# Kernel optimization log

Measured on AMD Instinct MI355X. Metric: run time of the kernel, lower is better.

## Reference

```python
import jax, jax.numpy as jnp
import numpy as np

D_MODEL = 1024
D_INNER = 2048  # expand * d_model
D_STATE = 16
D_CONV = 4
DT_RANK = 64    # ceil(d_model / 16)
B_SZ, L_SEQ = 2, 1024


def setup_inputs() -> dict:
    key = jax.random.key(0)
    ks = jax.random.split(key, 8)
    s = lambda fan_in: 1.0 / np.sqrt(fan_in)
    x = jax.random.normal(ks[0], (B_SZ, L_SEQ, D_MODEL), dtype=jnp.float32)
    in_proj_w = jax.random.normal(ks[1], (2 * D_INNER, D_MODEL), jnp.float32) * s(D_MODEL)
    conv_w = jax.random.normal(ks[2], (D_INNER, 1, D_CONV), jnp.float32) * s(D_CONV)
    conv_b = jax.random.normal(ks[3], (D_INNER,), jnp.float32) * 0.02
    x_proj_w = jax.random.normal(ks[4], (DT_RANK + 2 * D_STATE, D_INNER), jnp.float32) * s(D_INNER)
    dt_proj_w = jax.random.normal(ks[5], (D_INNER, DT_RANK), jnp.float32) * s(DT_RANK)
    dt_proj_b = jax.random.normal(ks[6], (D_INNER,), jnp.float32) * 0.02
    A_log = jnp.broadcast_to(jnp.log(jnp.arange(1, D_STATE + 1, dtype=jnp.float32)), (D_INNER, D_STATE))
    D_param = jnp.ones((D_INNER,), jnp.float32)
    out_proj_w = jax.random.normal(ks[7], (D_MODEL, D_INNER), jnp.float32) * s(D_INNER)
    return dict(x=x, in_proj_w=in_proj_w, conv_w=conv_w, conv_b=conv_b,
                x_proj_w=x_proj_w, dt_proj_w=dt_proj_w, dt_proj_b=dt_proj_b,
                A_log=A_log, D_param=D_param, out_proj_w=out_proj_w)


def _mamba_forward(x, in_proj_w, conv_w, conv_b, x_proj_w, dt_proj_w, dt_proj_b, A_log, D_param, out_proj_w):
    B, L, _ = x.shape
    # in_proj: (B,L,2*d_inner) -> split into conv branch and gate
    xz = jnp.einsum('bld,ed->ble', x, in_proj_w)
    x_br, z = jnp.split(xz, 2, axis=-1)
    # depthwise causal conv1d (left pad d_conv-1, truncate to L == torch pad+slice)
    xc = jnp.transpose(x_br, (0, 2, 1))  # (B, d_inner, L)
    xc = jax.lax.conv_general_dilated(
        xc, conv_w, window_strides=(1,), padding=[(D_CONV - 1, 0)],
        dimension_numbers=('NCH', 'OIH', 'NCH'), feature_group_count=D_INNER)
    xc = xc + conv_b[None, :, None]
    u = jax.nn.silu(jnp.transpose(xc, (0, 2, 1)))  # (B, L, d_inner) = SSM input
    # input-dependent params
    proj = jnp.einsum('bld,ed->ble', u, x_proj_w)
    delta_raw, B_in, C_in = jnp.split(proj, [DT_RANK, DT_RANK + D_STATE], axis=-1)
    delta = jax.nn.softplus(jnp.einsum('blr,dr->bld', delta_raw, dt_proj_w) + dt_proj_b)
    A = -jnp.exp(A_log)  # (d_inner, d_state)

    def step(h, inp):
        d_t, b_t, c_t, u_t = inp  # (B,d_inner),(B,d_state),(B,d_state),(B,d_inner)
        dA = jnp.exp(d_t[:, :, None] * A)                       # (B,d_inner,d_state)
        h = dA * h + (d_t * u_t)[:, :, None] * b_t[:, None, :]  # ZOH-ish update
        y_t = jnp.einsum('bds,bs->bd', h, c_t) + D_param * u_t
        return h, y_t

    h0 = jnp.zeros((B, D_INNER, D_STATE), dtype=x.dtype)
    inputs = (jnp.swapaxes(delta, 0, 1), jnp.swapaxes(B_in, 0, 1),
              jnp.swapaxes(C_in, 0, 1), jnp.swapaxes(u, 0, 1))
    _, ys = jax.lax.scan(step, h0, inputs)  # (L, B, d_inner)
    y = jnp.swapaxes(ys, 0, 1) * jax.nn.silu(z)
    return jnp.einsum('ble,de->bld', y, out_proj_w)


def reference(x, in_proj_w, conv_w, conv_b, x_proj_w, dt_proj_w, dt_proj_b, A_log, D_param, out_proj_w):
    return _mamba_forward(x, in_proj_w, conv_w, conv_b, x_proj_w, dt_proj_w, dt_proj_b, A_log, D_param, out_proj_w)
```

## Files before the change

kernel.cpp:

```cpp
#include <hip/hip_runtime.h>
#include <hip/hip_bf16.h>

#define D_MODEL 1024
#define D_INNER 2048
#define D_STATE 16
#define D_CONV  4
#define DT_RANK 64
#define B_SZ    2
#define L_SEQ   1024
#define BL      (B_SZ * L_SEQ)
#define NPROJ   (DT_RANK + 2 * D_STATE)

typedef __attribute__((ext_vector_type(8))) short bf16x8;
typedef __attribute__((ext_vector_type(4))) float floatx4;
typedef unsigned short ushort_t;

__device__ __forceinline__ void mfma_bf16(floatx4& acc, bf16x8 a, bf16x8 b) {
    asm volatile("v_mfma_f32_16x16x32_bf16 %0, %1, %2, %0"
                 : "+v"(acc) : "v"(a), "v"(b));
}

__device__ __forceinline__ void cvt_hilo(float f, ushort_t& hi, ushort_t& lo) {
    __hip_bfloat16 h = __float2bfloat16(f);
    hi = *(ushort_t*)&h;
    __hip_bfloat16 l = __float2bfloat16(f - __bfloat162float(h));
    lo = *(ushort_t*)&l;
}

__device__ __forceinline__ void cvt_store4(float4 v, ushort_t* hi, ushort_t* lo) {
    ushort4 h, l;
    cvt_hilo(v.x, h.x, l.x);
    cvt_hilo(v.y, h.y, l.y);
    cvt_hilo(v.z, h.z, l.z);
    cvt_hilo(v.w, h.w, l.w);
    *(ushort4*)hi = h;
    *(ushort4*)lo = l;
}

#define N4_WI 1048576
#define N4_WO 524288
#define N4_X  524288
#define N4_WD 32768
#define N4_TOT  (N4_WI + N4_WO + N4_X + N4_WD)

__global__ __launch_bounds__(256) void cvt_static(
    const float* __restrict__ wi, ushort_t* wihi, ushort_t* wilo,
    const float* __restrict__ wo, ushort_t* wohi, ushort_t* wolo,
    const float* __restrict__ x,  ushort_t* xhi,  ushort_t* xlo,
    const float* __restrict__ wd, ushort_t* wdhi, ushort_t* wdlo)
{
    int i = blockIdx.x * 256 + threadIdx.x;
    if (i >= N4_TOT) return;
    const float* src; ushort_t *dh, *dl;
    if (i < N4_WI)                 { src = wi; dh = wihi; dl = wilo; }
    else if ((i -= N4_WI) < N4_WO) { src = wo; dh = wohi; dl = wolo; }
    else if ((i -= N4_WO) < N4_X)  { src = x;  dh = xhi;  dl = xlo;  }
    else                           { i -= N4_X; src = wd; dh = wdhi; dl = wdlo; }
    float4 v = ((const float4*)src)[i];
    cvt_store4(v, dh + i * 4, dl + i * 4);
}

template <int KSPLIT>
__global__ __launch_bounds__(512, 1) void gemm_big(
    const ushort_t* __restrict__ Ahi, const ushort_t* __restrict__ Alo, int lda,
    const ushort_t* __restrict__ Bhi, const ushort_t* __restrict__ Blo, int ldb,
    float* __restrict__ C, int ldc, int K, size_t cslice)
{
    constexpr int BM = 128, BN = 256, LDT = 32;
    __shared__ __align__(16) ushort_t As[3][2][BM * LDT];
    __shared__ __align__(16) ushort_t Bs[3][2][BN * LDT];

    const int tid = threadIdx.x;
    const int bm = blockIdx.y * BM;
    const int bn = blockIdx.x * BN;
    const int kstart = (KSPLIT > 1) ? blockIdx.z * (K / KSPLIT) : 0;
    const int nt = ((KSPLIT > 1) ? K / KSPLIT : K) >> 5;

    const int wave = tid >> 6;
    const int lane = tid & 63;
    const int wm = (wave >> 2) * 64;
    const int wn = (wave & 3) * 64;
    const int ml = lane & 15;
    const int q  = lane >> 4;

    const int rsub = lane >> 2;
    const int gg   = ((lane & 3) ^ ((lane >> 3) & 3)) * 8;
    const ushort_t* gsrc = Ahi; int grow0 = bm, gld = lda;
    if (wave == 1)      { gsrc = Alo; grow0 = bm;       gld = lda; }
    else if (wave == 2) { gsrc = Bhi; grow0 = bn;       gld = ldb; }
    else if (wave == 3) { gsrc = Bhi; grow0 = bn + 128; gld = ldb; }
    else if (wave == 4) { gsrc = Blo; grow0 = bn;       gld = ldb; }
    else if (wave == 5) { gsrc = Blo; grow0 = bn + 128; gld = ldb; }
    const bool do_stage = (wave < 6);

    auto stage = [&](int buf, int kc) {
        if (!do_stage) return;
        ushort_t* lb;
        if (wave == 0)      lb = &As[buf][0][0];
        else if (wave == 1) lb = &As[buf][1][0];
        else if (wave == 2) lb = &Bs[buf][0][0];
        else if (wave == 3) lb = &Bs[buf][0][128 * LDT];
        else if (wave == 4) lb = &Bs[buf][1][0];
        else                lb = &Bs[buf][1][128 * LDT];
#pragma unroll
        for (int u2 = 0; u2 < 8; ++u2) {
            const int R0 = u2 * 16;
            const ushort_t* src =
                gsrc + (size_t)(grow0 + R0 + rsub) * gld + kc + gg;
            __builtin_amdgcn_global_load_lds(
                (const __attribute__((address_space(1))) unsigned int*)src,
                (__attribute__((address_space(3))) unsigned int*)(lb + R0 * LDT),
                16, 0, 0);
        }
    };

    floatx4 acc[4][4];
#pragma unroll
    for (int i = 0; i < 4; ++i)
#pragma unroll
        for (int j = 0; j < 4; ++j) acc[i][j] = (floatx4)0.f;

    stage(0, kstart);
    if (nt > 1) stage(1, kstart + 32);

    for (int t = 0; t < nt; ++t) {
        asm volatile("s_waitcnt vmcnt(8)" ::: "memory");
        __builtin_amdgcn_s_barrier();
        if (t + 2 < nt) stage((t + 2) % 3, kstart + ((t + 2) << 5));

        const int buf = t % 3;
        bf16x8 ah[4], al[4], bh[4], bl[4];
#pragma unroll
        for (int i = 0; i < 4; ++i) {
            const int r = wm + i * 16 + ml;
            const int p = (q ^ ((r >> 1) & 3)) * 8;
            ah[i] = *(const bf16x8*)&As[buf][0][r * LDT + p];
            al[i] = *(const bf16x8*)&As[buf][1][r * LDT + p];
        }
#pragma unroll
        for (int j = 0; j < 4; ++j) {
            const int r = wn + j * 16 + ml;
            const int p = (q ^ ((r >> 1) & 3)) * 8;
            bh[j] = *(const bf16x8*)&Bs[buf][0][r * LDT + p];
            bl[j] = *(const bf16x8*)&Bs[buf][1][r * LDT + p];
        }
#pragma unroll
        for (int i = 0; i < 4; ++i)
#pragma unroll
            for (int j = 0; j < 4; ++j) {
                mfma_bf16(acc[i][j], ah[i], bh[j]);
                mfma_bf16(acc[i][j], ah[i], bl[j]);
                mfma_bf16(acc[i][j], al[i], bh[j]);
            }
    }

    asm volatile("s_nop 7\n\ts_nop 7\n\ts_nop 7" ::: "memory");

    float* Cb = (KSPLIT > 1) ? C + (size_t)blockIdx.z * cslice : C;
#pragma unroll
    for (int i = 0; i < 4; ++i)
#pragma unroll
        for (int j = 0; j < 4; ++j)
#pragma unroll
            for (int r = 0; r < 4; ++r) {
                const int row = bm + wm + i * 16 + q * 4 + r;
                const int col = bn + wn + j * 16 + ml;
                Cb[(size_t)row * ldc + col] = acc[i][j][r];
            }
}

template <int TM, int TN, int EPI>
__global__ __launch_bounds__(256, 2) void gemm_pre(
    const ushort_t* __restrict__ Ahi, const ushort_t* __restrict__ Alo, int lda,
    const ushort_t* __restrict__ Bhi, const ushort_t* __restrict__ Blo, int ldb,
    float* __restrict__ C, int ldc, int K,
    const float* __restrict__ bias)
{
    static_assert(TM == 128 && TN == 128, "stage mapping assumes 128x128");
    constexpr int LDT = 32;
    constexpr int IT = TM / 32, JT = TN / 32;
    __shared__ __align__(16) ushort_t As[2][2][TM * LDT];
    __shared__ __align__(16) ushort_t Bs[2][2][TN * LDT];

    const int tid = threadIdx.x;
    const int bm = blockIdx.y * TM;
    const int bn = blockIdx.x * TN;

    const int wave = tid >> 6;
    const int lane = tid & 63;
    const int wm = (wave >> 1) * (TM / 2);
    const int wn = (wave & 1) * (TN / 2);
    const int ml = lane & 15;
    const int q  = lane >> 4;

    const ushort_t* gplane = (wave == 0) ? Ahi : (wave == 1) ? Alo
                           : (wave == 2) ? Bhi : Blo;
    const int grow0 = (wave < 2) ? bm : bn;
    const int gld   = (wave < 2) ? lda : ldb;
    const int rsub  = lane >> 2;
    const int gg    = ((lane & 3) ^ ((lane >> 3) & 3)) * 8;

    auto stage = [&](int buf, int kc) {
        ushort_t* lbase = (wave < 2) ? &As[buf][wave & 1][0]
                                     : &Bs[buf][wave & 1][0];
#pragma unroll
        for (int u = 0; u < 8; ++u) {
            const int R0 = u * 16;
            const ushort_t* src =
                gplane + (size_t)(grow0 + R0 + rsub) * gld + kc + gg;
            __builtin_amdgcn_global_load_lds(
                (const __attribute__((address_space(1))) unsigned int*)src,
                (__attribute__((address_space(3))) unsigned int*)(lbase + R0 * LDT),
                16, 0, 0);
        }
    };

    floatx4 acc[IT][JT];
#pragma unroll
    for (int i = 0; i < IT; ++i)
#pragma unroll
        for (int j = 0; j < JT; ++j) acc[i][j] = (floatx4)0.f;

    const int nt = K >> 5;

    stage(0, 0);
    __syncthreads();

    for (int t = 0; t < nt; ++t) {
        const int buf = t & 1;
        if (t + 1 < nt) stage(buf ^ 1, (t + 1) << 5);

        bf16x8 ah[IT], al[IT], bh[JT], bl[JT];
#pragma unroll
        for (int i = 0; i < IT; ++i) {
            const int r = wm + i * 16 + ml;
            const int p = (q ^ ((r >> 1) & 3)) * 8;
            ah[i] = *(const bf16x8*)&As[buf][0][r * LDT + p];
            al[i] = *(const bf16x8*)&As[buf][1][r * LDT + p];
        }
#pragma unroll
        for (int j = 0; j < JT; ++j) {
            const int r = wn + j * 16 + ml;
            const int p = (q ^ ((r >> 1) & 3)) * 8;
            bh[j] = *(const bf16x8*)&Bs[buf][0][r * LDT + p];
            bl[j] = *(const bf16x8*)&Bs[buf][1][r * LDT + p];
        }
#pragma unroll
        for (int i = 0; i < IT; ++i)
#pragma unroll
            for (int j = 0; j < JT; ++j) {
                mfma_bf16(acc[i][j], ah[i], bh[j]);
                mfma_bf16(acc[i][j], ah[i], bl[j]);
                mfma_bf16(acc[i][j], al[i], bh[j]);
            }

        __syncthreads();
    }

    asm volatile("s_nop 7\n\ts_nop 7\n\ts_nop 7" ::: "memory");

#pragma unroll
    for (int i = 0; i < IT; ++i)
#pragma unroll
        for (int j = 0; j < JT; ++j) {
            const int col = bn + wn + j * 16 + ml;
            const float bv = (EPI == 1) ? bias[col] : 0.f;
#pragma unroll
            for (int r = 0; r < 4; ++r) {
                const int row = bm + wm + i * 16 + q * 4 + r;
                float v = acc[i][j][r];
                if (EPI == 1) {
                    v += bv;
                    v = (v > 20.f) ? v : log1pf(__expf(v));
                }
                C[(size_t)row * ldc + col] = v;
            }
        }
}

__global__ __launch_bounds__(256) void fold_out(
    const float* __restrict__ s, float* __restrict__ out)
{
    const int i = blockIdx.x * 256 + threadIdx.x;
    const float4* s4 = (const float4*)s;
    constexpr int SL = BL * D_MODEL / 4;
    float4 a = s4[i], b = s4[i + SL], c = s4[i + 2 * SL], d = s4[i + 3 * SL];
    ((float4*)out)[i] = make_float4(a.x + b.x + c.x + d.x,
                                    a.y + b.y + c.y + d.y,
                                    a.z + b.z + c.z + d.z,
                                    a.w + b.w + c.w + d.w);
}

__global__ __launch_bounds__(256) void fold_proj(
    const float* __restrict__ pp, float* __restrict__ proj,
    ushort_t* __restrict__ Phi, ushort_t* __restrict__ Plo)
{
    const int i = blockIdx.x * 256 + threadIdx.x;
    constexpr int SL = BL * NPROJ / 4;
    float4 acc = make_float4(0.f, 0.f, 0.f, 0.f);
#pragma unroll
    for (int sp = 0; sp < 16; ++sp) {
        float4 v = ((const float4*)pp)[i + sp * SL];
        acc.x += v.x; acc.y += v.y; acc.z += v.z; acc.w += v.w;
    }
    ((float4*)proj)[i] = acc;

    const int row = i / (NPROJ / 4);
    const int c4  = i % (NPROJ / 4);
    if (c4 < DT_RANK / 4)
        cvt_store4(acc, Phi + (size_t)row * DT_RANK + c4 * 4,
                        Plo + (size_t)row * DT_RANK + c4 * 4);
}

#define PKC 128
#define PSC 64

__global__ __launch_bounds__(256) void gemm_proj_conv(
    const float* __restrict__ xz,
    const float* __restrict__ conv_w,
    const float* __restrict__ conv_b,
    const float* __restrict__ Wp,
    float* __restrict__ projp,
    float* __restrict__ u_out)
{
    __shared__ float us[PSC][65];
    __shared__ float wsh[PSC][100];

    const int tid = threadIdx.x;
    const int bm = blockIdx.y * 64;
    const int kbase0 = blockIdx.x * PKC;

    const int tx = tid & 15;
    const int ty = tid >> 4;

    float acc[4][6];
#pragma unroll
    for (int i = 0; i < 4; ++i)
#pragma unroll
        for (int j = 0; j < 6; ++j) acc[i][j] = 0.f;

    for (int sc = 0; sc < PKC / PSC; ++sc) {
        const int kb = kbase0 + sc * PSC;
        __syncthreads();
#pragma unroll
        for (int i = 0; i < 4; ++i) {
            const int flat = tid + 256 * i;
            const int r  = flat >> 4;
            const int kk = (flat & 15) * 4;
            const int k  = kb + kk;
            const int rr = bm + r;
            const int t  = rr & (L_SEQ - 1);
            const float* base = xz + (size_t)rr * 4096 + k;
            float4 x0 = *(const float4*)(base);
            float4 x1 = (t >= 1) ? *(const float4*)(base - 4096)  : make_float4(0,0,0,0);
            float4 x2 = (t >= 2) ? *(const float4*)(base - 8192)  : make_float4(0,0,0,0);
            float4 x3 = (t >= 3) ? *(const float4*)(base - 12288) : make_float4(0,0,0,0);
            float4 cb = *(const float4*)(conv_b + k);
            float4 w0 = ((const float4*)conv_w)[k + 0];
            float4 w1 = ((const float4*)conv_w)[k + 1];
            float4 w2 = ((const float4*)conv_w)[k + 2];
            float4 w3 = ((const float4*)conv_w)[k + 3];
            float4 uo;
            { float a = cb.x + w0.x*x3.x + w0.y*x2.x + w0.z*x1.x + w0.w*x0.x;
              uo.x = a / (1.f + __expf(-a)); }
            { float a = cb.y + w1.x*x3.y + w1.y*x2.y + w1.z*x1.y + w1.w*x0.y;
              uo.y = a / (1.f + __expf(-a)); }
            { float a = cb.z + w2.x*x3.z + w2.y*x2.z + w2.z*x1.z + w2.w*x0.z;
              uo.z = a / (1.f + __expf(-a)); }
            { float a = cb.w + w3.x*x3.w + w3.y*x2.w + w3.z*x1.w + w3.w*x0.w;
              uo.w = a / (1.f + __expf(-a)); }
            us[kk + 0][r] = uo.x;
            us[kk + 1][r] = uo.y;
            us[kk + 2][r] = uo.z;
            us[kk + 3][r] = uo.w;
            *(float4*)(u_out + (size_t)rr * D_INNER + k) = uo;
        }
#pragma unroll
        for (int i = 0; i < 6; ++i) {
            const int flat = tid + 256 * i;
            const int r = flat >> 4;
            const int k4 = flat & 15;
            float4 v = *(const float4*)(Wp + (size_t)r * D_INNER + kb + k4 * 4);
            wsh[k4*4+0][r] = v.x; wsh[k4*4+1][r] = v.y;
            wsh[k4*4+2][r] = v.z; wsh[k4*4+3][r] = v.w;
        }
        __syncthreads();

#pragma unroll 8
        for (int kk = 0; kk < PSC; ++kk) {
            float a[4], b[6];
#pragma unroll
            for (int i = 0; i < 4; ++i) a[i] = us[kk][ty * 4 + i];
#pragma unroll
            for (int j = 0; j < 6; ++j) b[j] = wsh[kk][tx + 16 * j];
#pragma unroll
            for (int i = 0; i < 4; ++i)
#pragma unroll
                for (int j = 0; j < 6; ++j) acc[i][j] += a[i] * b[j];
        }
    }

    float* pb = projp + (size_t)blockIdx.x * (BL * NPROJ);
#pragma unroll
    for (int i = 0; i < 4; ++i)
#pragma unroll
        for (int j = 0; j < 6; ++j)
            pb[(size_t)(bm + ty * 4 + i) * NPROJ + tx + 16 * j] = acc[i][j];
}

template <int CSv>
__global__ __launch_bounds__(256) void scan_phase_a(
    const float* __restrict__ xz,
    const float* __restrict__ u,
    const float* __restrict__ proj,
    const float* __restrict__ A_log,
    float* __restrict__ hloc,
    float* __restrict__ sumd,
    int nc)
{
    const int d = blockIdx.x * 256 + threadIdx.x;
    const int c = blockIdx.y;
    const int b = blockIdx.z;

    float a[D_STATE];
#pragma unroll
    for (int s = 0; s < D_STATE; ++s) a[s] = -__expf(A_log[d * D_STATE + s]);

    float h[D_STATE];
#pragma unroll
    for (int s = 0; s < D_STATE; ++s) h[s] = 0.f;
    float sd = 0.f;

    for (int t = c * CSv; t < (c + 1) * CSv; ++t) {
        const size_t bt = (size_t)b * L_SEQ + t;
        const float dv = xz[bt * (2 * D_INNER) + d];
        const float uv = u[bt * D_INNER + d];
        const float du = dv * uv;
        sd += dv;
        const float* pr = proj + bt * NPROJ;
#pragma unroll
        for (int s = 0; s < D_STATE; ++s)
            h[s] = __expf(dv * a[s]) * h[s] + du * pr[DT_RANK + s];
    }

    const size_t base = ((size_t)(b * nc + c) * D_STATE) * D_INNER + d;
#pragma unroll
    for (int s = 0; s < D_STATE; ++s) hloc[base + (size_t)s * D_INNER] = h[s];
    sumd[(size_t)(b * nc + c) * D_INNER + d] = sd;
}

__global__ __launch_bounds__(256) void scan_phase_b(
    const float* __restrict__ hloc,
    const float* __restrict__ sumd,
    const float* __restrict__ A_log,
    float* __restrict__ carry,
    int nc)
{
    const int g = blockIdx.x * 256 + threadIdx.x;
    const int d = g & (D_INNER - 1);
    const int s = (g >> 11) & (D_STATE - 1);
    const int b = g >> 15;

    const float a_s = -__expf(A_log[d * D_STATE + s]);

    float hc = 0.f;
    carry[((size_t)(b * nc + 0) * D_STATE + s) * D_INNER + d] = 0.f;

    for (int c = 1; c < nc; ++c) {
        const float sd = sumd[(size_t)(b * nc + c - 1) * D_INNER + d];
        const float hl = hloc[((size_t)(b * nc + c - 1) * D_STATE + s) * D_INNER + d];
        hc = __expf(a_s * sd) * hc + hl;
        carry[((size_t)(b * nc + c) * D_STATE + s) * D_INNER + d] = hc;
    }
}

template <int CSv>
__global__ __launch_bounds__(256) void scan_phase_c(
    const float* __restrict__ xz,
    const float* __restrict__ u,
    const float* __restrict__ proj,
    const float* __restrict__ A_log,
    const float* __restrict__ D_param,
    const float* __restrict__ carry,
    ushort_t* __restrict__ Yhi,
    ushort_t* __restrict__ Ylo,
    int nc)
{
    const int d = blockIdx.x * 256 + threadIdx.x;
    const int c = blockIdx.y;
    const int b = blockIdx.z;

    float a[D_STATE];
#pragma unroll
    for (int s = 0; s < D_STATE; ++s) a[s] = -__expf(A_log[d * D_STATE + s]);
    const float Dp = D_param[d];

    float h[D_STATE];
    const size_t cbase = ((size_t)(b * nc + c) * D_STATE) * D_INNER + d;
#pragma unroll
    for (int s = 0; s < D_STATE; ++s) h[s] = carry[cbase + (size_t)s * D_INNER];

    for (int t = c * CSv; t < (c + 1) * CSv; ++t) {
        const size_t bt = (size_t)b * L_SEQ + t;
        const float dv = xz[bt * (2 * D_INNER) + d];
        const float uv = u[bt * D_INNER + d];
        const float du = dv * uv;
        const float* pr = proj + bt * NPROJ;

        float acc = 0.f;
#pragma unroll
        for (int s = 0; s < D_STATE; ++s) {
            h[s] = __expf(dv * a[s]) * h[s] + du * pr[DT_RANK + s];
            acc += h[s] * pr[DT_RANK + D_STATE + s];
        }
        const float yv = acc + Dp * uv;

        const float zv = xz[bt * (2 * D_INNER) + D_INNER + d];
        const float gate = zv / (1.f + __expf(-zv));
        ushort_t hh, ll;
        cvt_hilo(yv * gate, hh, ll);
        Yhi[bt * D_INNER + d] = hh;
        Ylo[bt * D_INNER + d] = ll;
    }
}

extern "C" void kernel_launch(void* const* d_in, const int* in_sizes, int n_in,
                              void* d_out, int out_size, void* d_ws, size_t ws_size,
                              hipStream_t stream)
{
    const float* x         = (const float*)d_in[0];
    const float* in_proj_w = (const float*)d_in[1];
    const float* conv_w    = (const float*)d_in[2];
    const float* conv_b    = (const float*)d_in[3];
    const float* x_proj_w  = (const float*)d_in[4];
    const float* dt_proj_w = (const float*)d_in[5];
    const float* dt_proj_b = (const float*)d_in[6];
    const float* A_log     = (const float*)d_in[7];
    const float* D_param   = (const float*)d_in[8];
    const float* out_proj_w= (const float*)d_in[9];
    float* out = (float*)d_out;

    const size_t fixed =
        (size_t)BL * 4096 * 4 +
        (size_t)BL * 2048 * 4 +
        (size_t)BL * NPROJ * 4 +
        (size_t)(4096 + 2048) * 1024 * 2 * 2;
    const size_t need64 = fixed + (size_t)B_SZ * 64 * D_INNER * 4
                                + (size_t)B_SZ * 64 * D_STATE * D_INNER * 4;
    const int nc = (ws_size >= need64) ? 64 : 32;
    const int cs = L_SEQ / nc;

    float* xz    = (float*)d_ws;
    float* u     = xz    + (size_t)BL * 4096;
    float* proj  = u     + (size_t)BL * 2048;
    float* sumd  = proj  + (size_t)BL * NPROJ;
    float* carry = sumd  + (size_t)B_SZ * nc * D_INNER;
    ushort_t* Wihi = (ushort_t*)(carry + (size_t)B_SZ * nc * D_STATE * D_INNER);
    ushort_t* Wilo = Wihi + (size_t)4096 * 1024;
    ushort_t* Wohi = Wilo + (size_t)4096 * 1024;
    ushort_t* Wolo = Wohi + (size_t)1024 * 2048;
    ushort_t* Xhi  = (ushort_t*)carry;
    ushort_t* Xlo  = Xhi + (size_t)BL * D_MODEL;
    float*    hloc = (float*)Wihi;
    ushort_t* Yhi  = Wihi;
    ushort_t* Ylo  = Wilo;
    float*    projp = (float*)Wihi;
    ushort_t* Phi  = Xhi;
    ushort_t* Plo  = Xhi + (size_t)BL * DT_RANK;
    ushort_t* Wdhi = (ushort_t*)sumd;
    ushort_t* Wdlo = Wdhi + (size_t)D_INNER * DT_RANK;
    float*    Cslc  = xz;

    dim3 blk(256);
    dim3 blk512(512);

    cvt_static<<<(N4_TOT + 255) / 256, blk, 0, stream>>>(
        in_proj_w, Wihi, Wilo, out_proj_w, Wohi, Wolo, x, Xhi, Xlo,
        dt_proj_w, Wdhi, Wdlo);

    gemm_big<1><<<dim3(4096 / 256, BL / 128), blk512, 0, stream>>>(
        Xhi, Xlo, D_MODEL, Wihi, Wilo, D_MODEL, xz, 2 * D_INNER, D_MODEL, 0);

    gemm_proj_conv<<<dim3(D_INNER / PKC, BL / 64), blk, 0, stream>>>(
        xz, conv_w, conv_b, x_proj_w, projp, u);

    fold_proj<<<(BL * NPROJ / 4) / 256, blk, 0, stream>>>(projp, proj, Phi, Plo);

    gemm_pre<128, 128, 1><<<dim3(D_INNER / 128, BL / 128), blk, 0, stream>>>(
        Phi, Plo, DT_RANK, Wdhi, Wdlo, DT_RANK, xz, 2 * D_INNER, DT_RANK,
        dt_proj_b);

    if (cs == 16) {
        scan_phase_a<16><<<dim3(D_INNER / 256, nc, B_SZ), blk, 0, stream>>>(
            xz, u, proj, A_log, hloc, sumd, nc);
    } else {
        scan_phase_a<32><<<dim3(D_INNER / 256, nc, B_SZ), blk, 0, stream>>>(
            xz, u, proj, A_log, hloc, sumd, nc);
    }
    scan_phase_b<<<dim3((B_SZ * D_INNER * D_STATE) / 256), blk, 0, stream>>>(
        hloc, sumd, A_log, carry, nc);
    if (cs == 16) {
        scan_phase_c<16><<<dim3(D_INNER / 256, nc, B_SZ), blk, 0, stream>>>(
            xz, u, proj, A_log, D_param, carry, Yhi, Ylo, nc);
    } else {
        scan_phase_c<32><<<dim3(D_INNER / 256, nc, B_SZ), blk, 0, stream>>>(
            xz, u, proj, A_log, D_param, carry, Yhi, Ylo, nc);
    }

    gemm_big<4><<<dim3(D_MODEL / 256, BL / 128, 4), blk512, 0, stream>>>(
        Yhi, Ylo, D_INNER, Wohi, Wolo, D_INNER, Cslc, D_MODEL, D_INNER,
        (size_t)BL * D_MODEL);
    fold_out<<<(BL * D_MODEL / 4) / 256, blk, 0, stream>>>(Cslc, out);
}
```

Before: 295.0 us.

## Fuse dt_proj GEMM and softplus into scan phases, drop separate GEMM

Removes the split-bf16 dt_proj GEMM kernel, its weight and activation conversions, and the delta write to the xz buffer. Both scan phases now compute delta per thread in fp32 as a 64-wide dot product with dt_proj_w held in registers, then apply softplus. This saves a kernel launch and the delta round trip through global memory. In exchange the dt_proj matmul is done twice (in phase A and phase C) on plain FMA units, and register pressure rises (64 weights plus CSv deltas), with launch bounds set to 4 blocks per CU.

New measurement: 337.9 us. 1.15x slower.

```diff
diff --git a/kernel.cpp b/kernel.cpp
--- a/kernel.cpp
+++ b/kernel.cpp
@@ -40,22 +40,19 @@
 #define N4_WI 1048576
 #define N4_WO 524288
 #define N4_X  524288
-#define N4_WD 32768
-#define N4_TOT  (N4_WI + N4_WO + N4_X + N4_WD)
+#define N4_TOT  (N4_WI + N4_WO + N4_X)
 
 __global__ __launch_bounds__(256) void cvt_static(
     const float* __restrict__ wi, ushort_t* wihi, ushort_t* wilo,
     const float* __restrict__ wo, ushort_t* wohi, ushort_t* wolo,
-    const float* __restrict__ x,  ushort_t* xhi,  ushort_t* xlo,
-    const float* __restrict__ wd, ushort_t* wdhi, ushort_t* wdlo)
+    const float* __restrict__ x,  ushort_t* xhi,  ushort_t* xlo)
 {
     int i = blockIdx.x * 256 + threadIdx.x;
     if (i >= N4_TOT) return;
     const float* src; ushort_t *dh, *dl;
     if (i < N4_WI)                 { src = wi; dh = wihi; dl = wilo; }
     else if ((i -= N4_WI) < N4_WO) { src = wo; dh = wohi; dl = wolo; }
-    else if ((i -= N4_WO) < N4_X)  { src = x;  dh = xhi;  dl = xlo;  }
-    else                           { i -= N4_X; src = wd; dh = wdhi; dl = wdlo; }
+    else                           { i -= N4_WO; src = x; dh = xhi; dl = xlo; }
     float4 v = ((const float4*)src)[i];
     cvt_store4(v, dh + i * 4, dl + i * 4);
 }
@@ -169,115 +166,6 @@
             }
 }
 
-template <int TM, int TN, int EPI>
-__global__ __launch_bounds__(256, 2) void gemm_pre(
-    const ushort_t* __restrict__ Ahi, const ushort_t* __restrict__ Alo, int lda,
-    const ushort_t* __restrict__ Bhi, const ushort_t* __restrict__ Blo, int ldb,
-    float* __restrict__ C, int ldc, int K,
-    const float* __restrict__ bias)
-{
-    static_assert(TM == 128 && TN == 128, "stage mapping assumes 128x128");
-    constexpr int LDT = 32;
-    constexpr int IT = TM / 32, JT = TN / 32;
-    __shared__ __align__(16) ushort_t As[2][2][TM * LDT];
-    __shared__ __align__(16) ushort_t Bs[2][2][TN * LDT];
-
-    const int tid = threadIdx.x;
-    const int bm = blockIdx.y * TM;
-    const int bn = blockIdx.x * TN;
-
-    const int wave = tid >> 6;
-    const int lane = tid & 63;
-    const int wm = (wave >> 1) * (TM / 2);
-    const int wn = (wave & 1) * (TN / 2);
-    const int ml = lane & 15;
-    const int q  = lane >> 4;
-
-    const ushort_t* gplane = (wave == 0) ? Ahi : (wave == 1) ? Alo
-                           : (wave == 2) ? Bhi : Blo;
-    const int grow0 = (wave < 2) ? bm : bn;
-    const int gld   = (wave < 2) ? lda : ldb;
-    const int rsub  = lane >> 2;
-    const int gg    = ((lane & 3) ^ ((lane >> 3) & 3)) * 8;
-
-    auto stage = [&](int buf, int kc) {
-        ushort_t* lbase = (wave < 2) ? &As[buf][wave & 1][0]
-                                     : &Bs[buf][wave & 1][0];
-#pragma unroll
-        for (int u = 0; u < 8; ++u) {
-            const int R0 = u * 16;
-            const ushort_t* src =
-                gplane + (size_t)(grow0 + R0 + rsub) * gld + kc + gg;
-            __builtin_amdgcn_global_load_lds(
-                (const __attribute__((address_space(1))) unsigned int*)src,
-                (__attribute__((address_space(3))) unsigned int*)(lbase + R0 * LDT),
-                16, 0, 0);
-        }
-    };
-
-    floatx4 acc[IT][JT];
-#pragma unroll
-    for (int i = 0; i < IT; ++i)
-#pragma unroll
-        for (int j = 0; j < JT; ++j) acc[i][j] = (floatx4)0.f;
-
-    const int nt = K >> 5;
-
-    stage(0, 0);
-    __syncthreads();
-
-    for (int t = 0; t < nt; ++t) {
-        const int buf = t & 1;
-        if (t + 1 < nt) stage(buf ^ 1, (t + 1) << 5);
-
-        bf16x8 ah[IT], al[IT], bh[JT], bl[JT];
-#pragma unroll
-        for (int i = 0; i < IT; ++i) {
-            const int r = wm + i * 16 + ml;
-            const int p = (q ^ ((r >> 1) & 3)) * 8;
-            ah[i] = *(const bf16x8*)&As[buf][0][r * LDT + p];
-            al[i] = *(const bf16x8*)&As[buf][1][r * LDT + p];
-        }
-#pragma unroll
-        for (int j = 0; j < JT; ++j) {
-            const int r = wn + j * 16 + ml;
-            const int p = (q ^ ((r >> 1) & 3)) * 8;
-            bh[j] = *(const bf16x8*)&Bs[buf][0][r * LDT + p];
-            bl[j] = *(const bf16x8*)&Bs[buf][1][r * LDT + p];
-        }
-#pragma unroll
-        for (int i = 0; i < IT; ++i)
-#pragma unroll
-            for (int j = 0; j < JT; ++j) {
-                mfma_bf16(acc[i][j], ah[i], bh[j]);
-                mfma_bf16(acc[i][j], ah[i], bl[j]);
-                mfma_bf16(acc[i][j], al[i], bh[j]);
-            }
-
-        __syncthreads();
-    }
-
-    asm volatile("s_nop 7\n\ts_nop 7\n\ts_nop 7" ::: "memory");
-
-#pragma unroll
-    for (int i = 0; i < IT; ++i)
-#pragma unroll
-        for (int j = 0; j < JT; ++j) {
-            const int col = bn + wn + j * 16 + ml;
-            const float bv = (EPI == 1) ? bias[col] : 0.f;
-#pragma unroll
-            for (int r = 0; r < 4; ++r) {
-                const int row = bm + wm + i * 16 + q * 4 + r;
-                float v = acc[i][j][r];
-                if (EPI == 1) {
-                    v += bv;
-                    v = (v > 20.f) ? v : log1pf(__expf(v));
-                }
-                C[(size_t)row * ldc + col] = v;
-            }
-        }
-}
-
 __global__ __launch_bounds__(256) void fold_out(
     const float* __restrict__ s, float* __restrict__ out)
 {
@@ -292,8 +180,7 @@
 }
 
 __global__ __launch_bounds__(256) void fold_proj(
-    const float* __restrict__ pp, float* __restrict__ proj,
-    ushort_t* __restrict__ Phi, ushort_t* __restrict__ Plo)
+    const float* __restrict__ pp, float* __restrict__ proj)
 {
     const int i = blockIdx.x * 256 + threadIdx.x;
     constexpr int SL = BL * NPROJ / 4;
@@ -304,12 +191,6 @@
         acc.x += v.x; acc.y += v.y; acc.z += v.z; acc.w += v.w;
     }
     ((float4*)proj)[i] = acc;
-
-    const int row = i / (NPROJ / 4);
-    const int c4  = i % (NPROJ / 4);
-    if (c4 < DT_RANK / 4)
-        cvt_store4(acc, Phi + (size_t)row * DT_RANK + c4 * 4,
-                        Plo + (size_t)row * DT_RANK + c4 * 4);
 }
 
 #define PKC 128
@@ -409,10 +290,11 @@
 }
 
 template <int CSv>
-__global__ __launch_bounds__(256) void scan_phase_a(
-    const float* __restrict__ xz,
+__global__ __launch_bounds__(256, 4) void scan_phase_a(
     const float* __restrict__ u,
     const float* __restrict__ proj,
+    const float* __restrict__ Wd,
+    const float* __restrict__ dbias,
     const float* __restrict__ A_log,
     float* __restrict__ hloc,
     float* __restrict__ sumd,
@@ -422,6 +304,33 @@
     const int c = blockIdx.y;
     const int b = blockIdx.z;
 
+    float dloc[CSv];
+    float sd = 0.f;
+    {
+        float w[64];
+#pragma unroll
+        for (int k4 = 0; k4 < 16; ++k4) {
+            float4 v = *(const float4*)(Wd + (size_t)d * 64 + k4 * 4);
+            w[k4*4+0] = v.x; w[k4*4+1] = v.y; w[k4*4+2] = v.z; w[k4*4+3] = v.w;
+        }
+        const float bv = dbias[d];
+#pragma unroll
+        for (int tt = 0; tt < CSv; ++tt) {
+            const size_t bt = (size_t)b * L_SEQ + c * CSv + tt;
+            const float* pr = proj + bt * NPROJ;
+            float dr = bv;
+#pragma unroll
+            for (int k4 = 0; k4 < 16; ++k4) {
+                float4 p = *(const float4*)(pr + k4 * 4);
+                dr += p.x * w[k4*4+0] + p.y * w[k4*4+1]
+                    + p.z * w[k4*4+2] + p.w * w[k4*4+3];
+            }
+            const float dv = (dr > 20.f) ? dr : log1pf(__expf(dr));
+            dloc[tt] = dv;
+            sd += dv;
+        }
+    }
+
     float a[D_STATE];
 #pragma unroll
     for (int s = 0; s < D_STATE; ++s) a[s] = -__expf(A_log[d * D_STATE + s]);
@@ -429,14 +338,13 @@
     float h[D_STATE];
 #pragma unroll
     for (int s = 0; s < D_STATE; ++s) h[s] = 0.f;
-    float sd = 0.f;
-
-    for (int t = c * CSv; t < (c + 1) * CSv; ++t) {
-        const size_t bt = (size_t)b * L_SEQ + t;
-        const float dv = xz[bt * (2 * D_INNER) + d];
+
+#pragma unroll
+    for (int tt = 0; tt < CSv; ++tt) {
+        const size_t bt = (size_t)b * L_SEQ + c * CSv + tt;
+        const float dv = dloc[tt];
         const float uv = u[bt * D_INNER + d];
         const float du = dv * uv;
-        sd += dv;
         const float* pr = proj + bt * NPROJ;
 #pragma unroll
         for (int s = 0; s < D_STATE; ++s)
@@ -475,10 +383,12 @@
 }
 
 template <int CSv>
-__global__ __launch_bounds__(256) void scan_phase_c(
+__global__ __launch_bounds__(256, 4) void scan_phase_c(
     const float* __restrict__ xz,
     const float* __restrict__ u,
     const float* __restrict__ proj,
+    const float* __restrict__ Wd,
+    const float* __restrict__ dbias,
     const float* __restrict__ A_log,
     const float* __restrict__ D_param,
     const float* __restrict__ carry,
@@ -490,6 +400,30 @@
     const int c = blockIdx.y;
     const int b = blockIdx.z;
 
+    float dloc[CSv];
+    {
+        float w[64];
+#pragma unroll
+        for (int k4 = 0; k4 < 16; ++k4) {
+            float4 v = *(const float4*)(Wd + (size_t)d * 64 + k4 * 4);
+            w[k4*4+0] = v.x; w[k4*4+1] = v.y; w[k4*4+2] = v.z; w[k4*4+3] = v.w;
+        }
+        const float bv = dbias[d];
+#pragma unroll
+        for (int tt = 0; tt < CSv; ++tt) {
+            const size_t bt = (size_t)b * L_SEQ + c * CSv + tt;
+            const float* pr = proj + bt * NPROJ;
+            float dr = bv;
+#pragma unroll
+            for (int k4 = 0; k4 < 16; ++k4) {
+                float4 p = *(const float4*)(pr + k4 * 4);
+                dr += p.x * w[k4*4+0] + p.y * w[k4*4+1]
+                    + p.z * w[k4*4+2] + p.w * w[k4*4+3];
+            }
+            dloc[tt] = (dr > 20.f) ? dr : log1pf(__expf(dr));
+        }
+    }
+
     float a[D_STATE];
 #pragma unroll
     for (int s = 0; s < D_STATE; ++s) a[s] = -__expf(A_log[d * D_STATE + s]);
@@ -500,9 +434,10 @@
 #pragma unroll
     for (int s = 0; s < D_STATE; ++s) h[s] = carry[cbase + (size_t)s * D_INNER];
 
-    for (int t = c * CSv; t < (c + 1) * CSv; ++t) {
-        const size_t bt = (size_t)b * L_SEQ + t;
-        const float dv = xz[bt * (2 * D_INNER) + d];
+#pragma unroll
+    for (int tt = 0; tt < CSv; ++tt) {
+        const size_t bt = (size_t)b * L_SEQ + c * CSv + tt;
+        const float dv = dloc[tt];
         const float uv = u[bt * D_INNER + d];
         const float du = dv * uv;
         const float* pr = proj + bt * NPROJ;
@@ -565,18 +500,13 @@
     ushort_t* Yhi  = Wihi;
     ushort_t* Ylo  = Wilo;
     float*    projp = (float*)Wihi;
-    ushort_t* Phi  = Xhi;
-    ushort_t* Plo  = Xhi + (size_t)BL * DT_RANK;
-    ushort_t* Wdhi = (ushort_t*)sumd;
-    ushort_t* Wdlo = Wdhi + (size_t)D_INNER * DT_RANK;
     float*    Cslc  = xz;
 
     dim3 blk(256);
     dim3 blk512(512);
 
     cvt_static<<<(N4_TOT + 255) / 256, blk, 0, stream>>>(
-        in_proj_w, Wihi, Wilo, out_proj_w, Wohi, Wolo, x, Xhi, Xlo,
-        dt_proj_w, Wdhi, Wdlo);
+        in_proj_w, Wihi, Wilo, out_proj_w, Wohi, Wolo, x, Xhi, Xlo);
 
     gemm_big<1><<<dim3(4096 / 256, BL / 128), blk512, 0, stream>>>(
         Xhi, Xlo, D_MODEL, Wihi, Wilo, D_MODEL, xz, 2 * D_INNER, D_MODEL, 0);
@@ -584,27 +514,25 @@
     gemm_proj_conv<<<dim3(D_INNER / PKC, BL / 64), blk, 0, stream>>>(
         xz, conv_w, conv_b, x_proj_w, projp, u);
 
-    fold_proj<<<(BL * NPROJ / 4) / 256, blk, 0, stream>>>(projp, proj, Phi, Plo);
-
-    gemm_pre<128, 128, 1><<<dim3(D_INNER / 128, BL / 128), blk, 0, stream>>>(
-        Phi, Plo, DT_RANK, Wdhi, Wdlo, DT_RANK, xz, 2 * D_INNER, DT_RANK,
-        dt_proj_b);
+    fold_proj<<<(BL * NPROJ / 4) / 256, blk, 0, stream>>>(projp, proj);
 
     if (cs == 16) {
         scan_phase_a<16><<<dim3(D_INNER / 256, nc, B_SZ), blk, 0, stream>>>(
-            xz, u, proj, A_log, hloc, sumd, nc);
+            u, proj, dt_proj_w, dt_proj_b, A_log, hloc, sumd, nc);
     } else {
         scan_phase_a<32><<<dim3(D_INNER / 256, nc, B_SZ), blk, 0, stream>>>(
-            xz, u, proj, A_log, hloc, sumd, nc);
+            u, proj, dt_proj_w, dt_proj_b, A_log, hloc, sumd, nc);
     }
     scan_phase_b<<<dim3((B_SZ * D_INNER * D_STATE) / 256), blk, 0, stream>>>(
         hloc, sumd, A_log, carry, nc);
     if (cs == 16) {
         scan_phase_c<16><<<dim3(D_INNER / 256, nc, B_SZ), blk, 0, stream>>>(
-            xz, u, proj, A_log, D_param, carry, Yhi, Ylo, nc);
+            xz, u, proj, dt_proj_w, dt_proj_b, A_log, D_param, carry,
+            Yhi, Ylo, nc);
     } else {
         scan_phase_c<32><<<dim3(D_INNER / 256, nc, B_SZ), blk, 0, stream>>>(
-            xz, u, proj, A_log, D_param, carry, Yhi, Ylo, nc);
+            xz, u, proj, dt_proj_w, dt_proj_b, A_log, D_param, carry,
+            Yhi, Ylo, nc);
     }
 
     gemm_big<4><<<dim3(D_MODEL / 256, BL / 128, 4), blk512, 0, stream>>>(
```

## Split scan state dimension across two thread halves in scan phases A and C

Applied to the files above, without the earlier changes.

Phase A and phase C of the chunked selective scan now use 512-thread blocks, where each half handles 8 of the 16 state entries for the same channel. This doubles thread-level parallelism and halves the per-thread serial exp/FMA chain and register footprint. In phase C the two partial C·h sums are combined through shared memory after a barrier, and only one half does the gating and output writes. The cost is duplicated loads of delta/u per time step, an extra shared buffer, per-thread accumulator arrays sized by chunk length, and a sync.

New measurement: 383.2 us. +29.9%, slower.

```diff
diff --git a/kernel.cpp b/kernel.cpp
--- a/kernel.cpp
+++ b/kernel.cpp
@@ -409,7 +409,7 @@
 }
 
 template <int CSv>
-__global__ __launch_bounds__(256) void scan_phase_a(
+__global__ __launch_bounds__(512) void scan_phase_a(
     const float* __restrict__ xz,
     const float* __restrict__ u,
     const float* __restrict__ proj,
@@ -418,17 +418,18 @@
     float* __restrict__ sumd,
     int nc)
 {
-    const int d = blockIdx.x * 256 + threadIdx.x;
-    const int c = blockIdx.y;
-    const int b = blockIdx.z;
-
-    float a[D_STATE];
-#pragma unroll
-    for (int s = 0; s < D_STATE; ++s) a[s] = -__expf(A_log[d * D_STATE + s]);
-
-    float h[D_STATE];
-#pragma unroll
-    for (int s = 0; s < D_STATE; ++s) h[s] = 0.f;
+    const int dl = threadIdx.x & 255;
+    const int sg = threadIdx.x >> 8;
+    const int d  = blockIdx.x * 256 + dl;
+    const int c  = blockIdx.y;
+    const int b  = blockIdx.z;
+
+    float a[8], h[8];
+#pragma unroll
+    for (int s = 0; s < 8; ++s) {
+        a[s] = -__expf(A_log[d * D_STATE + sg * 8 + s]);
+        h[s] = 0.f;
+    }
     float sd = 0.f;
 
     for (int t = c * CSv; t < (c + 1) * CSv; ++t) {
@@ -437,16 +438,18 @@
         const float uv = u[bt * D_INNER + d];
         const float du = dv * uv;
         sd += dv;
-        const float* pr = proj + bt * NPROJ;
-#pragma unroll
-        for (int s = 0; s < D_STATE; ++s)
-            h[s] = __expf(dv * a[s]) * h[s] + du * pr[DT_RANK + s];
-    }
-
-    const size_t base = ((size_t)(b * nc + c) * D_STATE) * D_INNER + d;
-#pragma unroll
-    for (int s = 0; s < D_STATE; ++s) hloc[base + (size_t)s * D_INNER] = h[s];
-    sumd[(size_t)(b * nc + c) * D_INNER + d] = sd;
+        const float* pr = proj + bt * NPROJ + DT_RANK + sg * 8;
+#pragma unroll
+        for (int s = 0; s < 8; ++s)
+            h[s] = __expf(dv * a[s]) * h[s] + du * pr[s];
+    }
+
+    const size_t base =
+        ((size_t)(b * nc + c) * D_STATE + sg * 8) * D_INNER + d;
+#pragma unroll
+    for (int s = 0; s < 8; ++s) hloc[base + (size_t)s * D_INNER] = h[s];
+    if (sg == 0)
+        sumd[(size_t)(b * nc + c) * D_INNER + d] = sd;
 }
 
 __global__ __launch_bounds__(256) void scan_phase_b(
@@ -475,7 +478,7 @@
 }
 
 template <int CSv>
-__global__ __launch_bounds__(256) void scan_phase_c(
+__global__ __launch_bounds__(512) void scan_phase_c(
     const float* __restrict__ xz,
     const float* __restrict__ u,
     const float* __restrict__ proj,
@@ -486,41 +489,57 @@
     ushort_t* __restrict__ Ylo,
     int nc)
 {
-    const int d = blockIdx.x * 256 + threadIdx.x;
-    const int c = blockIdx.y;
-    const int b = blockIdx.z;
-
-    float a[D_STATE];
-#pragma unroll
-    for (int s = 0; s < D_STATE; ++s) a[s] = -__expf(A_log[d * D_STATE + s]);
-    const float Dp = D_param[d];
-
-    float h[D_STATE];
-    const size_t cbase = ((size_t)(b * nc + c) * D_STATE) * D_INNER + d;
-#pragma unroll
-    for (int s = 0; s < D_STATE; ++s) h[s] = carry[cbase + (size_t)s * D_INNER];
-
-    for (int t = c * CSv; t < (c + 1) * CSv; ++t) {
-        const size_t bt = (size_t)b * L_SEQ + t;
+    __shared__ float ys[CSv][256];
+    const int dl = threadIdx.x & 255;
+    const int sg = threadIdx.x >> 8;
+    const int d  = blockIdx.x * 256 + dl;
+    const int c  = blockIdx.y;
+    const int b  = blockIdx.z;
+
+    float a[8];
+#pragma unroll
+    for (int s = 0; s < 8; ++s)
+        a[s] = -__expf(A_log[d * D_STATE + sg * 8 + s]);
+
+    float h[8];
+    const size_t cbase =
+        ((size_t)(b * nc + c) * D_STATE + sg * 8) * D_INNER + d;
+#pragma unroll
+    for (int s = 0; s < 8; ++s) h[s] = carry[cbase + (size_t)s * D_INNER];
+
+    float acc_t[CSv];
+#pragma unroll
+    for (int tt = 0; tt < CSv; ++tt) {
+        const size_t bt = (size_t)b * L_SEQ + c * CSv + tt;
         const float dv = xz[bt * (2 * D_INNER) + d];
         const float uv = u[bt * D_INNER + d];
         const float du = dv * uv;
-        const float* pr = proj + bt * NPROJ;
-
+        const float* pr = proj + bt * NPROJ + DT_RANK;
         float acc = 0.f;
 #pragma unroll
-        for (int s = 0; s < D_STATE; ++s) {
-            h[s] = __expf(dv * a[s]) * h[s] + du * pr[DT_RANK + s];
-            acc += h[s] * pr[DT_RANK + D_STATE + s];
-        }
-        const float yv = acc + Dp * uv;
-
-        const float zv = xz[bt * (2 * D_INNER) + D_INNER + d];
-        const float gate = zv / (1.f + __expf(-zv));
-        ushort_t hh, ll;
-        cvt_hilo(yv * gate, hh, ll);
-        Yhi[bt * D_INNER + d] = hh;
-        Ylo[bt * D_INNER + d] = ll;
+        for (int s = 0; s < 8; ++s) {
+            h[s] = __expf(dv * a[s]) * h[s] + du * pr[sg * 8 + s];
+            acc += h[s] * pr[D_STATE + sg * 8 + s];
+        }
+        if (sg == 1) ys[tt][dl] = acc;
+        else         acc_t[tt] = acc;
+    }
+    __syncthreads();
+
+    if (sg == 0) {
+        const float Dp = D_param[d];
+#pragma unroll
+        for (int tt = 0; tt < CSv; ++tt) {
+            const size_t bt = (size_t)b * L_SEQ + c * CSv + tt;
+            const float uv = u[bt * D_INNER + d];
+            const float yv = acc_t[tt] + ys[tt][dl] + Dp * uv;
+            const float zv = xz[bt * (2 * D_INNER) + D_INNER + d];
+            const float gate = zv / (1.f + __expf(-zv));
+            ushort_t hh, ll;
+            cvt_hilo(yv * gate, hh, ll);
+            Yhi[bt * D_INNER + d] = hh;
+            Ylo[bt * D_INNER + d] = ll;
+        }
     }
 }
 
@@ -591,19 +610,19 @@
         dt_proj_b);
 
     if (cs == 16) {
-        scan_phase_a<16><<<dim3(D_INNER / 256, nc, B_SZ), blk, 0, stream>>>(
+        scan_phase_a<16><<<dim3(D_INNER / 256, nc, B_SZ), blk512, 0, stream>>>(
             xz, u, proj, A_log, hloc, sumd, nc);
     } else {
-        scan_phase_a<32><<<dim3(D_INNER / 256, nc, B_SZ), blk, 0, stream>>>(
+        scan_phase_a<32><<<dim3(D_INNER / 256, nc, B_SZ), blk512, 0, stream>>>(
             xz, u, proj, A_log, hloc, sumd, nc);
     }
     scan_phase_b<<<dim3((B_SZ * D_INNER * D_STATE) / 256), blk, 0, stream>>>(
         hloc, sumd, A_log, carry, nc);
     if (cs == 16) {
-        scan_phase_c<16><<<dim3(D_INNER / 256, nc, B_SZ), blk, 0, stream>>>(
+        scan_phase_c<16><<<dim3(D_INNER / 256, nc, B_SZ), blk512, 0, stream>>>(
             xz, u, proj, A_log, D_param, carry, Yhi, Ylo, nc);
     } else {
-        scan_phase_c<32><<<dim3(D_INNER / 256, nc, B_SZ), blk, 0, stream>>>(
+        scan_phase_c<32><<<dim3(D_INNER / 256, nc, B_SZ), blk512, 0, stream>>>(
             xz, u, proj, A_log, D_param, carry, Yhi, Ylo, nc);
     }
 
```
